# Optimization experiments

Measured on AMD Instinct MI355X. Metric: run time of the kernel, lower is better.

The kernel has to match this reference:

```python
import jax, jax.numpy as jnp
import numpy as np
from functools import partial

B, C, H, W = 16, 192, 32, 32
INNER, NH, DH, DCONV = 384, 12, 32, 4  # expand=2 -> INNER=2*C; 12 heads x 32 head_dim
S = H * W


def setup_inputs() -> dict:
    key = jax.random.key(0)
    ks = jax.random.split(key, 12)
    def n(k, shape, s=0.02):
        return jax.random.normal(k, shape, jnp.float32) * s
    f32 = jnp.float32
    return {
        "x": jax.random.normal(ks[0], (B, C, H, W), f32),
        "ln_w": jnp.ones((C,), f32), "ln_b": jnp.zeros((C,), f32),
        "w_up": n(ks[1], (C, 2 * INNER)), "b_up": jnp.zeros((2 * INNER,), f32),
        "conv_k": n(ks[2], (INNER, DCONV), 0.1), "conv_b": jnp.zeros((INNER,), f32),
        "w_q": n(ks[3], (INNER, INNER)), "w_k": n(ks[4], (INNER, INNER)),
        "w_i": n(ks[5], (3 * INNER, NH)), "b_i": jnp.zeros((NH,), f32),
        "w_f": n(ks[6], (3 * INNER, NH)), "b_f": 3.0 * jnp.ones((NH,), f32),
        "skip": jnp.ones((INNER,), f32),
        "mh_w": jnp.ones((INNER,), f32), "mh_b": jnp.zeros((INNER,), f32),
        "w_down": n(ks[7], (INNER, C)), "b_down": jnp.zeros((C,), f32),
        "w_lin": n(ks[8], (C, C)), "b_lin": jnp.zeros((C,), f32),
        "conv2_w": n(ks[9], (C, C, 3, 3), 0.05), "conv2_b": jnp.zeros((C,), f32),
        "bn_g": jnp.ones((C,), f32), "bn_b": jnp.zeros((C,), f32),
    }


def _layernorm(h, w, b, eps=1e-5):
    mu = h.mean(-1, keepdims=True)
    var = h.var(-1, keepdims=True)
    return (h - mu) / jnp.sqrt(var + eps) * w + b


def _mlstm_scan(q, k, v, i_pre, f_pre):
    # q,k,v: [B,S,NH,DH]; i_pre,f_pre: [B,S,NH]. Sequential matrix-memory mLSTM.
    qs, ks_, vs = (a.transpose(1, 0, 2, 3) for a in (q, k, v))  # seq-major
    iseq, fseq = i_pre.transpose(1, 0, 2), f_pre.transpose(1, 0, 2)

    def step(carry, inp):
        Cst, nst, mst = carry            # [B,NH,DH,DH], [B,NH,DH], [B,NH]
        qt, kt, vt, it, ft = inp
        log_f = jax.nn.log_sigmoid(ft)
        m_new = jnp.maximum(log_f + mst, it)
        f_s = jnp.exp(log_f + mst - m_new)[..., None]   # [B,NH,1]
        i_s = jnp.exp(it - m_new)[..., None]
        C_new = f_s[..., None] * Cst + i_s[..., None] * (vt[..., :, None] * kt[..., None, :])
        n_new = f_s * nst + i_s * kt
        denom = jnp.maximum(jnp.abs(jnp.einsum('bhd,bhd->bh', n_new, qt)), 1.0)[..., None]
        h = jnp.einsum('bhde,bhe->bhd', C_new, qt) / denom
        return (C_new, n_new, m_new), h

    bsz = q.shape[0]
    carry0 = (jnp.zeros((bsz, NH, DH, DH), q.dtype),
              jnp.zeros((bsz, NH, DH), q.dtype),
              jnp.zeros((bsz, NH), q.dtype))
    _, hs = jax.lax.scan(step, carry0, (qs, ks_, vs, iseq, fseq))
    return hs.transpose(1, 0, 2, 3)  # [B,S,NH,DH]


def _vil_block(seq, ln_w, ln_b, w_up, b_up, conv_k, conv_b, w_q, w_k,
               w_i, b_i, w_f, b_f, skip, mh_w, mh_b, w_down, b_down):
    # seq: [B,S,C]. Pre-norm mLSTM block (ViLBlock, rowwise-from-top-left order).
    bsz, s = seq.shape[0], seq.shape[1]
    h = _layernorm(seq, ln_w, ln_b)
    x_in, z = jnp.split(h @ w_up + b_up, 2, axis=-1)       # [B,S,INNER] each
    # causal depthwise conv1d, kernel DCONV
    x_pad = jnp.pad(x_in, ((0, 0), (DCONV - 1, 0), (0, 0)))
    x_conv = sum(x_pad[:, t:t + s, :] * conv_k[:, t] for t in range(DCONV)) + conv_b
    x_act = jax.nn.silu(x_conv)
    q = x_act @ w_q
    k = x_act @ w_k
    v = x_in
    gin = jnp.concatenate([q, k, v], -1)                    # [B,S,3*INNER]
    i_pre = gin @ w_i + b_i                                  # [B,S,NH]
    f_pre = gin @ w_f + b_f
    qh = q.reshape(bsz, s, NH, DH)
    kh = k.reshape(bsz, s, NH, DH) * (DH ** -0.5)
    vh = v.reshape(bsz, s, NH, DH)
    hs = _mlstm_scan(qh, kh, vh, i_pre, f_pre)              # [B,S,NH,DH]
    # per-head group norm
    mu = hs.mean(-1, keepdims=True)
    var = hs.var(-1, keepdims=True)
    hn = ((hs - mu) / jnp.sqrt(var + 1e-5)).reshape(bsz, s, INNER) * mh_w + mh_b
    h_out = (hn + skip * x_act) * jax.nn.silu(z)
    return seq + (h_out @ w_down + b_down)


def reference(x, ln_w, ln_b, w_up, b_up, conv_k, conv_b, w_q, w_k, w_i, b_i,
              w_f, b_f, skip, mh_w, mh_b, w_down, b_down, w_lin, b_lin,
              conv2_w, conv2_b, bn_g, bn_b):
    bsz, c, hh, ww = x.shape
    seq = x.reshape(bsz, c, hh * ww).transpose(0, 2, 1)     # [B,S,C]
    x1 = _vil_block(seq, ln_w, ln_b, w_up, b_up, conv_k, conv_b, w_q, w_k,
                    w_i, b_i, w_f, b_f, skip, mh_w, mh_b, w_down, b_down)
    x1 = x1.transpose(0, 2, 1).reshape(bsz, c, hh, ww)
    x2 = jax.nn.silu(seq @ w_lin + b_lin).transpose(0, 2, 1).reshape(bsz, c, hh, ww)
    y = x1 + x2
    y = jax.lax.conv_general_dilated(y, conv2_w, (1, 1), ((1, 1), (1, 1)),
                                     dimension_numbers=('NCHW', 'OIHW', 'NCHW'))
    y = y + conv2_b[None, :, None, None]
    # BatchNorm2d, training mode (batch statistics, biased variance)
    mu = y.mean((0, 2, 3), keepdims=True)
    var = y.var((0, 2, 3), keepdims=True)
    y = (y - mu) / jnp.sqrt(var + 1e-5) * bn_g[None, :, None, None] + bn_b[None, :, None, None]
    return jnp.where(y >= 0, y, 0.01 * y)  # LeakyReLU(0.01)
```

## Files before the change

kernel.cpp:

```cpp
#include <hip/hip_runtime.h>
#include <hip/hip_bf16.h>

#define BATCH 16
#define CDIM  192
#define SDIM  1024
#define INNER 384
#define NHEAD 12
#define DHEAD 32
#define UPN   768

typedef unsigned short ushort_t;
typedef __attribute__((ext_vector_type(8))) short bf16x8;
typedef __attribute__((ext_vector_type(4))) float f32x4;

__device__ __forceinline__ float us2f(ushort_t u) {
  union { unsigned int i; float f; } x; x.i = ((unsigned int)u) << 16; return x.f;
}
__device__ __forceinline__ float bits2f(unsigned int i) {
  union { unsigned int i; float f; } x; x.i = i; return x.f;
}
__device__ __forceinline__ ushort_t f2us(float f) {
  union { float f; unsigned int i; } x; x.f = f;
  unsigned int lsb = (x.i >> 16) & 1u;
  x.i += 0x7fffu + lsb;
  return (ushort_t)(x.i >> 16);
}
__device__ __forceinline__ void unpack8(uint4 u, float* o) {
  o[0] = bits2f(u.x << 16); o[1] = bits2f(u.x & 0xffff0000u);
  o[2] = bits2f(u.y << 16); o[3] = bits2f(u.y & 0xffff0000u);
  o[4] = bits2f(u.z << 16); o[5] = bits2f(u.z & 0xffff0000u);
  o[6] = bits2f(u.w << 16); o[7] = bits2f(u.w & 0xffff0000u);
}

__global__ void detect_kernel(const ushort_t* __restrict__ ln_w_raw,
                              int* __restrict__ flag) {
  if (threadIdx.x == 0) flag[0] = (ln_w_raw[0] == 0x3F80) ? 0 : 1;
}

#define NSEG 23
#define CANON_TOTAL 917600
struct CvtArgs { const void* src[NSEG]; };
__global__ __launch_bounds__(256) void convert_kernel(
    CvtArgs args, ushort_t* __restrict__ canon, const int* __restrict__ flagp) {
  const int offs[NSEG + 1] = {0, 192, 384, 147840, 148608, 150144, 150528,
      297984, 445440, 459264, 459280, 473104, 473120, 473504, 473888, 474272,
      548000, 548192, 585056, 585248, 917024, 917216, 917408, CANON_TOTAL};
  const int cnts[NSEG] = {192, 192, 147456, 768, 1536, 384, 147456, 147456,
      13824, 12, 13824, 12, 384, 384, 384, 73728, 192, 36864, 192, 331776,
      192, 192, 192};
  const int segK[NSEG] = {0,0,192,0,0,0,384,384,1152,0,1152,0,0,0,0,384,0,192,0,0,0,0,0};
  const int segN[NSEG] = {0,0,768,0,0,0,384,384,12,0,12,0,0,0,0,192,0,192,0,0,0,0,0};
  int idx = blockIdx.x * 256 + threadIdx.x;
  if (idx >= CANON_TOTAL) return;
  bool f32 = (*flagp) != 0;
  int seg = 0;
#pragma unroll
  for (int i = 1; i < NSEG; ++i) if (idx >= offs[i]) seg = i;
  int local = idx - offs[seg];
  ushort_t v = 0;
  if (local < cnts[seg]) {
    int srcidx = local;
    if (segK[seg] > 0) {
      int K = segK[seg], N = segN[seg];
      int n = local / K, k = local - n * K;
      srcidx = k * N + n;
    } else if (seg == 19) {
      int uv = local / 36864;
      int rem = local - uv * 36864;
      int co = rem / 192, ci = rem - co * 192;
      srcidx = (co * 192 + ci) * 9 + uv;
    }
    if (f32) v = f2us(((const float*)args.src[seg])[srcidx]);
    else     v = ((const ushort_t*)args.src[seg])[srcidx];
  }
  canon[idx] = v;
}

#define C_LN_W   0
#define C_LN_B   192
#define C_W_UP   384
#define C_B_UP   147840
#define C_CONV_K 148608
#define C_CONV_B 150144
#define C_W_Q    150528
#define C_W_K    297984
#define C_W_I    445440
#define C_B_I    459264
#define C_W_F    459280
#define C_B_F    473104
#define C_SKIP   473120
#define C_MH_W   473504
#define C_MH_B   473888
#define C_W_DOWN 474272
#define C_B_DOWN 548000
#define C_W_LIN  548192
#define C_B_LIN  585056
#define C_CONV2W 585248
#define C_CONV2B 917024
#define C_BN_G   917216
#define C_BN_B   917408

__global__ __launch_bounds__(256) void transpose_in_kernel(
    const void* __restrict__ xraw, ushort_t* __restrict__ seq,
    const int* __restrict__ flagp) {
  __shared__ ushort_t tile[32][33];
  bool f32 = (*flagp) != 0;
  int b = blockIdx.z, s0 = blockIdx.y * 32, c0 = blockIdx.x * 32;
  int tx = threadIdx.x, ty = threadIdx.y;
#pragma unroll
  for (int i = 0; i < 4; ++i) {
    int c = c0 + ty + i * 8;
    size_t idx = ((size_t)b * CDIM + c) * SDIM + s0 + tx;
    tile[ty + i * 8][tx] = f32 ? f2us(((const float*)xraw)[idx])
                               : ((const ushort_t*)xraw)[idx];
  }
  __syncthreads();
#pragma unroll
  for (int i = 0; i < 4; ++i) {
    int s = s0 + ty + i * 8;
    seq[((size_t)b * SDIM + s) * CDIM + c0 + tx] = tile[tx][ty + i * 8];
  }
}

__global__ __launch_bounds__(64) void ln_kernel(
    const ushort_t* __restrict__ seq, const ushort_t* __restrict__ w,
    const ushort_t* __restrict__ bias, ushort_t* __restrict__ hln) {
  size_t row = blockIdx.x;
  int lane = threadIdx.x;
  const ushort_t* p = seq + row * CDIM;
  float x0 = us2f(p[lane]), x1 = us2f(p[lane + 64]), x2 = us2f(p[lane + 128]);
  float s = x0 + x1 + x2;
#pragma unroll
  for (int off = 1; off <= 32; off <<= 1) s += __shfl_xor(s, off, 64);
  float mu = s * (1.0f / 192.0f);
  float d0 = x0 - mu, d1 = x1 - mu, d2 = x2 - mu;
  float sq = d0 * d0 + d1 * d1 + d2 * d2;
#pragma unroll
  for (int off = 1; off <= 32; off <<= 1) sq += __shfl_xor(sq, off, 64);
  float inv = rsqrtf(sq * (1.0f / 192.0f) + 1e-5f);
  ushort_t* o = hln + row * CDIM;
  o[lane]       = f2us(d0 * inv * us2f(w[lane])       + us2f(bias[lane]));
  o[lane + 64]  = f2us(d1 * inv * us2f(w[lane + 64])  + us2f(bias[lane + 64]));
  o[lane + 128] = f2us(d2 * inv * us2f(w[lane + 128]) + us2f(bias[lane + 128]));
}

#define GBK 32
#define LPAD 8
__global__ __launch_bounds__(256) void gemm_mfma(
    const ushort_t* __restrict__ A, int K,
    const ushort_t* __restrict__ Bt,
    float* Cf, ushort_t* Cb, int N,
    const ushort_t* __restrict__ bias,
    const ushort_t* add_bf, const float* add_f, int mode) {
  __shared__ ushort_t As[64][GBK + LPAD];
  __shared__ ushort_t Bs[64][GBK + LPAD];
  int tid = threadIdx.x;
  int wave = tid >> 6, lane = tid & 63;
  int m0 = blockIdx.y * 64, n0 = blockIdx.x * 64;
  int lr = tid >> 2;
  int lk = (tid & 3) * 8;
  int fr = lane & 15;
  int kq = (lane >> 4) * 8;
  f32x4 acc[4];
#pragma unroll
  for (int nt = 0; nt < 4; ++nt) acc[nt] = (f32x4){0.f, 0.f, 0.f, 0.f};
  const ushort_t* Ap = A + (size_t)(m0 + lr) * K + lk;
  const ushort_t* Bp = Bt + (size_t)(n0 + lr) * K + lk;
  for (int k0 = 0; k0 < K; k0 += GBK) {
    *(uint4*)&As[lr][lk] = *(const uint4*)(Ap + k0);
    *(uint4*)&Bs[lr][lk] = *(const uint4*)(Bp + k0);
    __syncthreads();
    bf16x8 af = *(const bf16x8*)&As[wave * 16 + fr][kq];
#pragma unroll
    for (int nt = 0; nt < 4; ++nt) {
      bf16x8 bf = *(const bf16x8*)&Bs[nt * 16 + fr][kq];
      acc[nt] = __builtin_amdgcn_mfma_f32_16x16x32_bf16(af, bf, acc[nt], 0, 0, 0);
    }
    __syncthreads();
  }
#pragma unroll
  for (int nt = 0; nt < 4; ++nt) {
    int col = n0 + nt * 16 + fr;
    float bv = bias ? us2f(bias[col]) : 0.0f;
#pragma unroll
    for (int r = 0; r < 4; ++r) {
      int row = m0 + wave * 16 + ((lane >> 4) << 2) + r;
      float v = acc[nt][r] + bv;
      if (mode == 1) {
        v = v / (1.0f + expf(-v));
      } else if (mode == 2) {
        size_t off = (size_t)row * N + col;
        v += us2f(add_bf[off]) + add_f[off];
      }
      if (Cb) Cb[(size_t)row * N + col] = f2us(v);
      else    Cf[(size_t)row * N + col] = v;
    }
  }
}

__global__ __launch_bounds__(256) void conv3_mfma_kernel(
    const ushort_t* __restrict__ ybsc, const ushort_t* __restrict__ w2t,
    const ushort_t* __restrict__ cbias, float* __restrict__ convo) {
  __shared__ ushort_t As[64][GBK + LPAD];
  __shared__ ushort_t Bs[64][GBK + LPAD];
  int tid = threadIdx.x;
  int wave = tid >> 6, lane = tid & 63;
  int n0 = blockIdx.x * 64;
  int my = blockIdx.y;
  int b = my >> 4;
  int m0 = (my & 15) * 64;
  int lr = tid >> 2, lk = (tid & 3) * 8;
  int fr = lane & 15, kq = (lane >> 4) * 8;
  f32x4 acc[4];
#pragma unroll
  for (int nt = 0; nt < 4; ++nt) acc[nt] = (f32x4){0.f, 0.f, 0.f, 0.f};
  int p = m0 + lr;
  int pi = p >> 5, pj = p & 31;
  const size_t brow = (size_t)b * SDIM;
#pragma unroll
  for (int uv = 0; uv < 9; ++uv) {
    int du = uv / 3 - 1, dv = uv % 3 - 1;
    bool valid = (pi + du >= 0) && (pi + du < 32) && (pj + dv >= 0) && (pj + dv < 32);
    const ushort_t* Ap = ybsc + (brow + p + du * 32 + dv) * CDIM + lk;
    const ushort_t* Bp = w2t + (size_t)uv * 36864 + (size_t)(n0 + lr) * CDIM + lk;
    for (int k0 = 0; k0 < CDIM; k0 += GBK) {
      uint4 av = {0u, 0u, 0u, 0u};
      if (valid) av = *(const uint4*)(Ap + k0);
      *(uint4*)&As[lr][lk] = av;
      *(uint4*)&Bs[lr][lk] = *(const uint4*)(Bp + k0);
      __syncthreads();
      bf16x8 af = *(const bf16x8*)&As[wave * 16 + fr][kq];
#pragma unroll
      for (int nt = 0; nt < 4; ++nt) {
        bf16x8 bf = *(const bf16x8*)&Bs[nt * 16 + fr][kq];
        acc[nt] = __builtin_amdgcn_mfma_f32_16x16x32_bf16(af, bf, acc[nt], 0, 0, 0);
      }
      __syncthreads();
    }
  }
#pragma unroll
  for (int nt = 0; nt < 4; ++nt) {
    int col = n0 + nt * 16 + fr;
    float bv = us2f(cbias[col]);
#pragma unroll
    for (int r = 0; r < 4; ++r) {
      int row = m0 + wave * 16 + ((lane >> 4) << 2) + r;
      convo[(brow + row) * CDIM + col] = acc[nt][r] + bv;
    }
  }
}

__global__ __launch_bounds__(256) void dwconv_kernel(
    const ushort_t* __restrict__ UPb, const ushort_t* __restrict__ ck,
    const ushort_t* __restrict__ cb, ushort_t* __restrict__ xact) {
  int idx = blockIdx.x * 256 + threadIdx.x;
  int ch = idx % INNER;
  int s = (idx / INNER) % SDIM;
  int b = idx / (INNER * SDIM);
  const ushort_t* p = UPb + ((size_t)b * SDIM + s) * UPN + ch;
  float acc = us2f(cb[ch]);
#pragma unroll
  for (int t = 0; t < 4; ++t) {
    int sp = s - 3 + t;
    if (sp >= 0) acc += us2f(p[(long)(t - 3) * UPN]) * us2f(ck[ch * 4 + t]);
  }
  xact[((size_t)b * SDIM + s) * INNER + ch] = f2us(acc / (1.0f + expf(-acc)));
}

__global__ __launch_bounds__(256) void gates_mfma_kernel(
    const ushort_t* __restrict__ qb, const ushort_t* __restrict__ kb,
    const ushort_t* __restrict__ UPb,
    const ushort_t* __restrict__ wiT, const ushort_t* __restrict__ b_i,
    const ushort_t* __restrict__ wfT, const ushort_t* __restrict__ b_f,
    float* __restrict__ ipre, float* __restrict__ fpre) {
  __shared__ ushort_t As[64][GBK + LPAD];
  __shared__ ushort_t Bs[32][GBK + LPAD];
  int tid = threadIdx.x;
  int wave = tid >> 6, lane = tid & 63;
  int m0 = blockIdx.x * 64;
  int lr = tid >> 2, lk = (tid & 3) * 8;
  int bn = tid >> 3, bk = (tid & 7) * 4;
  int fr = lane & 15, kq = (lane >> 4) * 8;
  f32x4 acc0 = (f32x4){0.f, 0.f, 0.f, 0.f};
  f32x4 acc1 = (f32x4){0.f, 0.f, 0.f, 0.f};
  for (int k0 = 0; k0 < 3 * INNER; k0 += GBK) {
    int reg = k0 / INNER;
    int off = k0 - reg * INNER + lk;
    const ushort_t* Ap;
    if (reg == 0)      Ap = qb + (size_t)(m0 + lr) * INNER + off;
    else if (reg == 1) Ap = kb + (size_t)(m0 + lr) * INNER + off;
    else               Ap = UPb + (size_t)(m0 + lr) * UPN + off;
    *(uint4*)&As[lr][lk] = *(const uint4*)Ap;
    ushort4 bv = {0, 0, 0, 0};
    if (bn < 12)       bv = *(const ushort4*)(wiT + (size_t)bn * 1152 + k0 + bk);
    else if (bn < 24)  bv = *(const ushort4*)(wfT + (size_t)(bn - 12) * 1152 + k0 + bk);
    *(ushort4*)&Bs[bn][bk] = bv;
    __syncthreads();
    bf16x8 af = *(const bf16x8*)&As[wave * 16 + fr][kq];
    bf16x8 bf0 = *(const bf16x8*)&Bs[fr][kq];
    acc0 = __builtin_amdgcn_mfma_f32_16x16x32_bf16(af, bf0, acc0, 0, 0, 0);
    bf16x8 bf1 = *(const bf16x8*)&Bs[16 + fr][kq];
    acc1 = __builtin_amdgcn_mfma_f32_16x16x32_bf16(af, bf1, acc1, 0, 0, 0);
    __syncthreads();
  }
#pragma unroll
  for (int r = 0; r < 4; ++r) {
    int row = m0 + wave * 16 + ((lane >> 4) << 2) + r;
    {
      int col = fr;
      float v = acc0[r];
      if (col < 12)      ipre[(size_t)row * NHEAD + col] = v + us2f(b_i[col]);
      else               fpre[(size_t)row * NHEAD + col - 12] = v + us2f(b_f[col - 12]);
    }
    {
      int col = 16 + fr;
      if (col < 24) fpre[(size_t)row * NHEAD + col - 12] = acc1[r] + us2f(b_f[col - 12]);
    }
  }
}

#define CHL 64
#define SAST 72

__global__ __launch_bounds__(256) void scanA_kernel(
    const ushort_t* __restrict__ qb, const ushort_t* __restrict__ kb,
    const ushort_t* __restrict__ UPb,
    const float* __restrict__ ipre, const float* __restrict__ fpre,
    ushort_t* __restrict__ hs, float* __restrict__ srowG,
    float* __restrict__ MlocG, float* __restrict__ sumG,
    ushort_t* __restrict__ CdG, ushort_t* __restrict__ ndG) {
  __shared__ ushort_t Qs[64 * SAST];
  __shared__ ushort_t Ks[64 * SAST];
  __shared__ ushort_t KtS[32 * SAST];
  __shared__ ushort_t VtS[48 * SAST];
  __shared__ ushort_t VwS[48 * SAST];
  __shared__ ushort_t Ss[64 * SAST];
  __shared__ float garr[CHL], Mloc_s[CHL], wlk_s[CHL];

  const int bx = blockIdx.x;
  const int bh = bx >> 4, c = bx & 15;
  const int b = bh / NHEAD, h = bh % NHEAD;
  const int tid = threadIdx.x;
  const int lane = tid & 63, wave = tid >> 6;
  const int quad = lane >> 4, fr = lane & 15;
  const int kq = quad * 8;
  const float kscale = 0.17677669529663687f;
  const size_t base384 = (size_t)b * SDIM * INNER + h * DHEAD;
  const size_t base768 = (size_t)b * SDIM * UPN + h * DHEAD;
  const size_t gbase = (size_t)b * SDIM * NHEAD + h;

  const int u = tid >> 2, dd0 = (tid & 3) * 8;
  size_t rb = base384 + (size_t)(c * CHL + u) * INNER + dd0;
  uint4 qv = *(const uint4*)(qb + rb);
  uint4 kv = *(const uint4*)(kb + rb);
  uint4 vv = *(const uint4*)(UPb + base768 + (size_t)(c * CHL + u) * UPN + dd0);
  *(uint4*)&Qs[u * SAST + dd0] = qv;
  *(uint4*)&Ks[u * SAST + dd0] = kv;
  {
    unsigned int words[4] = {kv.x, kv.y, kv.z, kv.w};
#pragma unroll
    for (int i = 0; i < 4; ++i) {
      KtS[(dd0 + 2 * i) * SAST + u] = (ushort_t)(words[i] & 0xffffu);
      KtS[(dd0 + 2 * i + 1) * SAST + u] = (ushort_t)(words[i] >> 16);
    }
  }
  if (tid < CHL) VtS[32 * SAST + tid] = 0x3F80;
  if (wave == 0) {
    float fv = fpre[gbase + (size_t)(c * CHL + lane) * NHEAD];
    float iv = ipre[gbase + (size_t)(c * CHL + lane) * NHEAD];
    float lf = fminf(fv, 0.0f) - log1pf(expf(-fabsf(fv)));
    float A = lf;
#pragma unroll
    for (int off = 1; off <= 32; off <<= 1) {
      float nb = __shfl_up(A, off, 64);
      if (lane >= off) A += nb;
    }
    float g = iv - A;
    float Mg = g;
#pragma unroll
    for (int off = 1; off <= 32; off <<= 1) {
      float nb = __shfl_up(Mg, off, 64);
      if (lane >= off) Mg = fmaxf(Mg, nb);
    }
    float Mg63 = __shfl(Mg, 63, 64);
    garr[lane] = g;
    Mloc_s[lane] = Mg;
    wlk_s[lane] = expf(g - Mg63) * kscale;
    MlocG[bx * CHL + lane] = Mg;
    if (lane == 63) { sumG[2 * bx] = A; sumG[2 * bx + 1] = Mg; }
  }
  __syncthreads();

  {
    float wk = wlk_s[u];
    unsigned int words[4] = {vv.x, vv.y, vv.z, vv.w};
#pragma unroll
    for (int i = 0; i < 4; ++i) {
      ushort_t lo = (ushort_t)(words[i] & 0xffffu);
      ushort_t hi = (ushort_t)(words[i] >> 16);
      VtS[(dd0 + 2 * i) * SAST + u] = lo;
      VtS[(dd0 + 2 * i + 1) * SAST + u] = hi;
      VwS[(dd0 + 2 * i) * SAST + u] = f2us(us2f(lo) * wk);
      VwS[(dd0 + 2 * i + 1) * SAST + u] = f2us(us2f(hi) * wk);
    }
    if (tid < CHL) VwS[32 * SAST + tid] = f2us(wlk_s[tid]);
  }
  f32x4 accS[4];
  {
    bf16x8 af = *(const bf16x8*)&Qs[(wave * 16 + fr) * SAST + kq];
#pragma unroll
    for (int nt = 0; nt < 4; ++nt) {
      bf16x8 bf = *(const bf16x8*)&Ks[(nt * 16 + fr) * SAST + kq];
      accS[nt] = __builtin_amdgcn_mfma_f32_16x16x32_bf16(
          af, bf, (f32x4){0.f, 0.f, 0.f, 0.f}, 0, 0, 0);
    }
  }
  {
    float Mls[4];
#pragma unroll
    for (int r = 0; r < 4; ++r) Mls[r] = Mloc_s[wave * 16 + quad * 4 + r];
#pragma unroll
    for (int nt = 0; nt < 4; ++nt) {
      int uu = nt * 16 + fr;
      float gu = garr[uu];
#pragma unroll
      for (int r = 0; r < 4; ++r) {
        int t = wave * 16 + quad * 4 + r;
        float sv = (uu <= t) ? accS[nt][r] * kscale * expf(gu - Mls[r]) : 0.0f;
        Ss[t * SAST + uu] = f2us(sv);
      }
    }
  }
  __syncthreads();

  f32x4 acc2[3];
#pragma unroll
  for (int nt = 0; nt < 3; ++nt) acc2[nt] = (f32x4){0.f, 0.f, 0.f, 0.f};
#pragma unroll
  for (int ks = 0; ks < 2; ++ks) {
    bf16x8 af = *(const bf16x8*)&Ss[(wave * 16 + fr) * SAST + kq + 32 * ks];
#pragma unroll
    for (int nt = 0; nt < 3; ++nt) {
      bf16x8 bf = *(const bf16x8*)&VtS[(nt * 16 + fr) * SAST + kq + 32 * ks];
      acc2[nt] = __builtin_amdgcn_mfma_f32_16x16x32_bf16(af, bf, acc2[nt], 0, 0, 0);
    }
  }
  f32x4 accC[2];
  const int nC = (wave < 2) ? 2 : 1;
#pragma unroll
  for (int tt = 0; tt < 2; ++tt) {
    if (tt < nC) {
      int tix = wave + tt * 4;
      int m = tix >> 1, n = tix & 1;
      f32x4 a = (f32x4){0.f, 0.f, 0.f, 0.f};
#pragma unroll
      for (int ks = 0; ks < 2; ++ks) {
        bf16x8 af = *(const bf16x8*)&VwS[(m * 16 + fr) * SAST + kq + 32 * ks];
        bf16x8 bf = *(const bf16x8*)&KtS[(n * 16 + fr) * SAST + kq + 32 * ks];
        a = __builtin_amdgcn_mfma_f32_16x16x32_bf16(af, bf, a, 0, 0, 0);
      }
      accC[tt] = a;
    }
  }
#pragma unroll
  for (int r = 0; r < 4; ++r) {
    int t = wave * 16 + quad * 4 + r;
    size_t hrow = base384 + (size_t)(c * CHL + t) * INNER;
    hs[hrow + fr] = f2us(acc2[0][r]);
    hs[hrow + 16 + fr] = f2us(acc2[1][r]);
    if (fr == 0) srowG[bx * CHL + t] = acc2[2][r];
  }
#pragma unroll
  for (int tt = 0; tt < 2; ++tt) {
    if (tt < nC) {
      int tix = wave + tt * 4;
      int m = tix >> 1, n = tix & 1;
#pragma unroll
      for (int r = 0; r < 4; ++r) {
        int dp = m * 16 + quad * 4 + r;
        int e = n * 16 + fr;
        if (dp < 32)       CdG[(size_t)bx * 1024 + dp * 32 + e] = f2us(accC[tt][r]);
        else if (dp == 32) ndG[bx * 32 + e] = f2us(accC[tt][r]);
      }
    }
  }
}

__global__ __launch_bounds__(256) void scanB_kernel(
    ushort_t* __restrict__ CdG, ushort_t* __restrict__ ndG,
    float* __restrict__ sumG) {
  __shared__ float Cl[DHEAD][33];
  __shared__ float nl[DHEAD];
  const int bh = blockIdx.x;
  const int tid = threadIdx.x;
  const int d = tid & 31, e0 = tid >> 5;
  Cl[d][e0] = 0.0f; Cl[d][e0 + 8] = 0.0f;
  Cl[d][e0 + 16] = 0.0f; Cl[d][e0 + 24] = 0.0f;
  if (tid < DHEAD) nl[tid] = 0.0f;
  float m = 0.0f;
  __syncthreads();
  for (int c = 0; c < 16; ++c) {
    int bx = bh * 16 + c;
    float A63 = sumG[2 * bx], Mg63 = sumG[2 * bx + 1];
    ushort_t* Cd = CdG + (size_t)bx * 1024 + d * 32;
    float d0 = us2f(Cd[e0]), d1 = us2f(Cd[e0 + 8]);
    float d2 = us2f(Cd[e0 + 16]), d3 = us2f(Cd[e0 + 24]);
    float ndel = (tid < DHEAD) ? us2f(ndG[bx * 32 + tid]) : 0.0f;
    __syncthreads();
    Cd[e0] = f2us(Cl[d][e0]); Cd[e0 + 8] = f2us(Cl[d][e0 + 8]);
    Cd[e0 + 16] = f2us(Cl[d][e0 + 16]); Cd[e0 + 24] = f2us(Cl[d][e0 + 24]);
    if (tid < DHEAD) ndG[bx * 32 + tid] = f2us(nl[tid]);
    if (tid == 0) sumG[2 * bx] = m;
    float M63 = fmaxf(m, Mg63);
    float al = expf(m - M63), sc = expf(Mg63 - M63);
    Cl[d][e0] = al * Cl[d][e0] + sc * d0;
    Cl[d][e0 + 8] = al * Cl[d][e0 + 8] + sc * d1;
    Cl[d][e0 + 16] = al * Cl[d][e0 + 16] + sc * d2;
    Cl[d][e0 + 24] = al * Cl[d][e0 + 24] + sc * d3;
    if (tid < DHEAD) nl[tid] = al * nl[tid] + sc * ndel;
    m = A63 + M63;
    __syncthreads();
  }
}

__global__ __launch_bounds__(256) void scanC_kernel(
    const ushort_t* __restrict__ qb, const ushort_t* __restrict__ CdG,
    const ushort_t* __restrict__ ndG, const float* __restrict__ sumG,
    const float* __restrict__ srowG, const float* __restrict__ MlocG,
    ushort_t* __restrict__ hs) {
  __shared__ ushort_t Qs[64 * SAST];
  __shared__ ushort_t Bs2[48 * 40];
  __shared__ float als[CHL], scs[CHL], rden[CHL];
  __shared__ float mprev_s;
  const int bx = blockIdx.x;
  const int bh = bx >> 4, c = bx & 15;
  const int b = bh / NHEAD, h = bh % NHEAD;
  const int tid = threadIdx.x;
  const int lane = tid & 63, wave = tid >> 6;
  const int quad = lane >> 4, fr = lane & 15;
  const int kq = quad * 8;
  const size_t base384 = (size_t)b * SDIM * INNER + h * DHEAD;
  {
    int u = tid >> 2, dd0 = (tid & 3) * 8;
    size_t rb = base384 + (size_t)(c * CHL + u) * INNER + dd0;
    *(uint4*)&Qs[u * SAST + dd0] = *(const uint4*)(qb + rb);
  }
  if (tid < 128) {
    int d = tid >> 2, e0 = (tid & 3) * 8;
    *(uint4*)&Bs2[d * 40 + e0] =
        *(const uint4*)(CdG + (size_t)bx * 1024 + d * 32 + e0);
  } else if (tid < 160) {
    Bs2[32 * 40 + (tid - 128)] = ndG[bx * 32 + (tid - 128)];
  } else if (tid == 160) {
    mprev_s = sumG[2 * bx];
  }
  __syncthreads();
  f32x4 acc[3];
  {
    bf16x8 af = *(const bf16x8*)&Qs[(wave * 16 + fr) * SAST + kq];
#pragma unroll
    for (int nt = 0; nt < 3; ++nt) {
      bf16x8 bf = *(const bf16x8*)&Bs2[(nt * 16 + fr) * 40 + kq];
      acc[nt] = __builtin_amdgcn_mfma_f32_16x16x32_bf16(
          af, bf, (f32x4){0.f, 0.f, 0.f, 0.f}, 0, 0, 0);
    }
  }
  float mp = mprev_s;
  if (fr == 0) {
#pragma unroll
    for (int r = 0; r < 4; ++r) {
      int t = wave * 16 + quad * 4 + r;
      float Mloc = MlocG[bx * CHL + t];
      float srow = srowG[bx * CHL + t];
      float Mt = fmaxf(mp, Mloc);
      float al = expf(mp - Mt), sc = expf(Mloc - Mt);
      float ndot = al * acc[2][r] + sc * srow;
      als[t] = al; scs[t] = sc;
      rden[t] = 1.0f / fmaxf(fabsf(ndot), 1.0f);
    }
  }
  __syncthreads();
#pragma unroll
  for (int r = 0; r < 4; ++r) {
    int t = wave * 16 + quad * 4 + r;
    float al = als[t], sc = scs[t], rd = rden[t];
    size_t hrow = base384 + (size_t)(c * CHL + t) * INNER;
#pragma unroll
    for (int nt = 0; nt < 2; ++nt) {
      size_t off = hrow + nt * 16 + fr;
      float intra = us2f(hs[off]);
      hs[off] = f2us((al * acc[nt][r] + sc * intra) * rd);
    }
  }
}

__global__ __launch_bounds__(384) void gnorm_kernel(
    ushort_t* __restrict__ hs, const ushort_t* __restrict__ xact,
    const ushort_t* __restrict__ UPb, const ushort_t* __restrict__ mh_w,
    const ushort_t* __restrict__ mh_b, const ushort_t* __restrict__ skip) {
  size_t row = blockIdx.x;
  int t = threadIdx.x;
  float val = us2f(hs[row * INNER + t]);
  float s = val;
#pragma unroll
  for (int off = 1; off <= 16; off <<= 1) s += __shfl_xor(s, off, 64);
  float mu = s * (1.0f / 32.0f);
  float d = val - mu;
  float sq = d * d;
#pragma unroll
  for (int off = 1; off <= 16; off <<= 1) sq += __shfl_xor(sq, off, 64);
  float var = sq * (1.0f / 32.0f);
  float hn = d * rsqrtf(var + 1e-5f) * us2f(mh_w[t]) + us2f(mh_b[t]);
  float xa = us2f(xact[row * INNER + t]);
  float z = us2f(UPb[row * UPN + INNER + t]);
  float sz = z / (1.0f + expf(-z));
  hs[row * INNER + t] = f2us((hn + us2f(skip[t]) * xa) * sz);
}

__global__ __launch_bounds__(192) void bnpart_kernel(
    const float* __restrict__ convo, float* __restrict__ part) {
  int blk = blockIdx.x;
  int c = threadIdx.x;
  float s = 0.0f, s2 = 0.0f;
  const float* p = convo + (size_t)blk * 64 * CDIM + c;
  for (int r = 0; r < 64; ++r) {
    float v = p[(size_t)r * CDIM];
    s += v; s2 += v * v;
  }
  part[blk * 384 + c] = s;
  part[blk * 384 + 192 + c] = s2;
}

__global__ __launch_bounds__(192) void bnreduce_kernel(
    const float* __restrict__ part, float* __restrict__ stats) {
  int c = threadIdx.x;
  double s = 0.0, s2 = 0.0;
  for (int b = 0; b < 256; ++b) {
    s += (double)part[b * 384 + c];
    s2 += (double)part[b * 384 + 192 + c];
  }
  double mu = s * (1.0 / 16384.0);
  double var = s2 * (1.0 / 16384.0) - mu * mu;
  if (var < 0.0) var = 0.0;
  stats[2 * c] = (float)mu;
  stats[2 * c + 1] = (float)(1.0 / sqrt(var + 1e-5));
}

__global__ __launch_bounds__(256) void bnapply_t_kernel(
    const float* __restrict__ convo, const float* __restrict__ stats,
    const ushort_t* __restrict__ g, const ushort_t* __restrict__ bb,
    void* __restrict__ out, const int* __restrict__ flagp) {
  __shared__ float tile[32][33];
  int b = blockIdx.z, s0 = blockIdx.y * 32, c0 = blockIdx.x * 32;
  int tx = threadIdx.x, ty = threadIdx.y;
  int c = c0 + tx;
  float mu = stats[2 * c], inv = stats[2 * c + 1];
  float gg = us2f(g[c]), bv = us2f(bb[c]);
#pragma unroll
  for (int i = 0; i < 4; ++i) {
    int s = s0 + ty + i * 8;
    float v = convo[((size_t)b * SDIM + s) * CDIM + c];
    v = (v - mu) * inv * gg + bv;
    v = v >= 0.0f ? v : 0.01f * v;
    tile[ty + i * 8][tx] = v;
  }
  __syncthreads();
  bool f32o = (*flagp) != 0;
#pragma unroll
  for (int i = 0; i < 4; ++i) {
    int cc = c0 + ty + i * 8;
    float v = tile[tx][ty + i * 8];
    size_t oidx = ((size_t)b * CDIM + cc) * SDIM + s0 + tx;
    if (f32o) ((float*)out)[oidx] = v;
    else      ((ushort_t*)out)[oidx] = f2us(v);
  }
}

extern "C" void kernel_launch(void* const* d_in, const int* in_sizes, int n_in,
                              void* d_out, int out_size, void* d_ws, size_t ws_size,
                              hipStream_t stream) {
  (void)in_sizes; (void)n_in; (void)out_size; (void)ws_size;
  char* w = (char*)d_ws;
  ushort_t* seqb  = (ushort_t*)(w + 0);
  ushort_t* hlnb  = (ushort_t*)(w + 6291456);
  ushort_t* UPb   = (ushort_t*)(w + 12582912);
  ushort_t* xactb = (ushort_t*)(w + 37748736);
  ushort_t* qbb   = (ushort_t*)(w + 50331648);
  ushort_t* kbb   = (ushort_t*)(w + 62914560);
  ushort_t* hsb   = (ushort_t*)(w + 75497472);
  float* ipre     = (float*)(w + 88080384);
  float* fpre     = (float*)(w + 88866816);
  float* stats    = (float*)(w + 89653248);
  int* flag       = (int*)(w + 89654784);
  ushort_t* canon = (ushort_t*)(w + 89654848);
  float* srowG    = (float*)(w + 91490048);
  float* MlocG    = (float*)(w + 92276480);
  float* sumG     = (float*)(w + 93062912);
  ushort_t* CdG   = (ushort_t*)(w + 93087488);
  ushort_t* ndG   = (ushort_t*)(w + 99378944);
  float* x2f      = (float*)xactb;
  ushort_t* ybscb = hlnb;
  float* convo    = (float*)qbb;
  float* part     = (float*)kbb;

  const ushort_t* ln_w   = canon + C_LN_W;
  const ushort_t* ln_b   = canon + C_LN_B;
  const ushort_t* w_upT  = canon + C_W_UP;
  const ushort_t* b_up   = canon + C_B_UP;
  const ushort_t* conv_k = canon + C_CONV_K;
  const ushort_t* conv_b = canon + C_CONV_B;
  const ushort_t* w_qT   = canon + C_W_Q;
  const ushort_t* w_kT   = canon + C_W_K;
  const ushort_t* w_iT   = canon + C_W_I;
  const ushort_t* b_i    = canon + C_B_I;
  const ushort_t* w_fT   = canon + C_W_F;
  const ushort_t* b_f    = canon + C_B_F;
  const ushort_t* skip   = canon + C_SKIP;
  const ushort_t* mh_w   = canon + C_MH_W;
  const ushort_t* mh_b   = canon + C_MH_B;
  const ushort_t* w_downT= canon + C_W_DOWN;
  const ushort_t* b_down = canon + C_B_DOWN;
  const ushort_t* w_linT = canon + C_W_LIN;
  const ushort_t* b_lin  = canon + C_B_LIN;
  const ushort_t* conv2w = canon + C_CONV2W;
  const ushort_t* conv2b = canon + C_CONV2B;
  const ushort_t* bn_g   = canon + C_BN_G;
  const ushort_t* bn_b   = canon + C_BN_B;

  detect_kernel<<<1, 64, 0, stream>>>((const ushort_t*)d_in[1], flag);
  CvtArgs ca;
  for (int i = 0; i < NSEG; ++i) ca.src[i] = d_in[i + 1];
  convert_kernel<<<(CANON_TOTAL + 255) / 256, 256, 0, stream>>>(ca, canon, flag);

  transpose_in_kernel<<<dim3(6, 32, 16), dim3(32, 8), 0, stream>>>(d_in[0], seqb, flag);
  ln_kernel<<<16384, 64, 0, stream>>>(seqb, ln_w, ln_b, hlnb);
  gemm_mfma<<<dim3(12, 256), 256, 0, stream>>>(hlnb, CDIM, w_upT, nullptr, UPb,
                                               UPN, b_up, nullptr, nullptr, 0);
  dwconv_kernel<<<24576, 256, 0, stream>>>(UPb, conv_k, conv_b, xactb);
  gemm_mfma<<<dim3(6, 256), 256, 0, stream>>>(xactb, INNER, w_qT, nullptr, qbb,
                                              INNER, nullptr, nullptr, nullptr, 0);
  gemm_mfma<<<dim3(6, 256), 256, 0, stream>>>(xactb, INNER, w_kT, nullptr, kbb,
                                              INNER, nullptr, nullptr, nullptr, 0);
  gates_mfma_kernel<<<256, 256, 0, stream>>>(qbb, kbb, UPb, w_iT, b_i, w_fT, b_f,
                                             ipre, fpre);
  scanA_kernel<<<3072, 256, 0, stream>>>(qbb, kbb, UPb, ipre, fpre, hsb,
                                         srowG, MlocG, sumG, CdG, ndG);
  scanB_kernel<<<192, 256, 0, stream>>>(CdG, ndG, sumG);
  scanC_kernel<<<3072, 256, 0, stream>>>(qbb, CdG, ndG, sumG, srowG, MlocG, hsb);
  gnorm_kernel<<<16384, 384, 0, stream>>>(hsb, xactb, UPb, mh_w, mh_b, skip);
  gemm_mfma<<<dim3(3, 256), 256, 0, stream>>>(seqb, CDIM, w_linT, x2f, nullptr,
                                              CDIM, b_lin, nullptr, nullptr, 1);
  gemm_mfma<<<dim3(3, 256), 256, 0, stream>>>(hsb, INNER, w_downT, nullptr, ybscb,
                                              CDIM, b_down, seqb, x2f, 2);
  conv3_mfma_kernel<<<dim3(3, 256), 256, 0, stream>>>(ybscb, conv2w, conv2b, convo);
  bnpart_kernel<<<256, 192, 0, stream>>>(convo, part);
  bnreduce_kernel<<<1, 192, 0, stream>>>(part, stats);
  bnapply_t_kernel<<<dim3(6, 32, 16), dim3(32, 8), 0, stream>>>(convo, stats, bn_g,
                                                                bn_b, d_out, flag);
}
```

Before: 390.4 us.

## Fuse Q/K GEMMs, fold group-norm into scanC, merge lin and down GEMMs

Three fusions. The separate Q and K projection GEMMs become one launch that splits output columns between the two buffers. The per-row head group-norm, skip and SiLU gating move into scanC's epilogue using shuffle reductions, which removes the gnorm kernel and its extra read/write of hs. The SiLU linear branch and the down projection are computed in one kernel with two accumulators, which removes the fp32 x2f intermediate buffer. The Q/K fusion assumes w_q and w_k are stored contiguously in the canonical weight buffer.

Measured after the change: 364.9 us. -6.5%, faster.

```diff
diff --git a/kernel.cpp b/kernel.cpp
--- a/kernel.cpp
+++ b/kernel.cpp
@@ -149,9 +149,8 @@
 __global__ __launch_bounds__(256) void gemm_mfma(
     const ushort_t* __restrict__ A, int K,
     const ushort_t* __restrict__ Bt,
-    float* Cf, ushort_t* Cb, int N,
-    const ushort_t* __restrict__ bias,
-    const ushort_t* add_bf, const float* add_f, int mode) {
+    ushort_t* Cb, ushort_t* Cb2, int splitN, int N,
+    const ushort_t* __restrict__ bias) {
   __shared__ ushort_t As[64][GBK + LPAD];
   __shared__ ushort_t Bs[64][GBK + LPAD];
   int tid = threadIdx.x;
@@ -182,18 +181,78 @@
   for (int nt = 0; nt < 4; ++nt) {
     int col = n0 + nt * 16 + fr;
     float bv = bias ? us2f(bias[col]) : 0.0f;
+    ushort_t* dst = Cb;
+    int c2 = col;
+    if (col >= splitN) { dst = Cb2; c2 = col - splitN; }
 #pragma unroll
     for (int r = 0; r < 4; ++r) {
       int row = m0 + wave * 16 + ((lane >> 4) << 2) + r;
-      float v = acc[nt][r] + bv;
-      if (mode == 1) {
-        v = v / (1.0f + expf(-v));
-      } else if (mode == 2) {
-        size_t off = (size_t)row * N + col;
-        v += us2f(add_bf[off]) + add_f[off];
+      dst[(size_t)row * N + c2] = f2us(acc[nt][r] + bv);
+    }
+  }
+}
+
+__global__ __launch_bounds__(256) void gemm_lindown(
+    const ushort_t* __restrict__ seq, const ushort_t* __restrict__ hsb,
+    const ushort_t* __restrict__ wlinT, const ushort_t* __restrict__ b_lin,
+    const ushort_t* __restrict__ wdownT, const ushort_t* __restrict__ b_down,
+    ushort_t* __restrict__ out) {
+  __shared__ ushort_t As[64][GBK + LPAD];
+  __shared__ ushort_t Bs[64][GBK + LPAD];
+  int tid = threadIdx.x;
+  int wave = tid >> 6, lane = tid & 63;
+  int m0 = blockIdx.y * 64, n0 = blockIdx.x * 64;
+  int lr = tid >> 2, lk = (tid & 3) * 8;
+  int fr = lane & 15, kq = (lane >> 4) * 8;
+  f32x4 accL[4], accD[4];
+#pragma unroll
+  for (int nt = 0; nt < 4; ++nt) {
+    accL[nt] = (f32x4){0.f, 0.f, 0.f, 0.f};
+    accD[nt] = (f32x4){0.f, 0.f, 0.f, 0.f};
+  }
+  {
+    const ushort_t* Ap = seq + (size_t)(m0 + lr) * CDIM + lk;
+    const ushort_t* Bp = wlinT + (size_t)(n0 + lr) * CDIM + lk;
+    for (int k0 = 0; k0 < CDIM; k0 += GBK) {
+      *(uint4*)&As[lr][lk] = *(const uint4*)(Ap + k0);
+      *(uint4*)&Bs[lr][lk] = *(const uint4*)(Bp + k0);
+      __syncthreads();
+      bf16x8 af = *(const bf16x8*)&As[wave * 16 + fr][kq];
+#pragma unroll
+      for (int nt = 0; nt < 4; ++nt) {
+        bf16x8 bf = *(const bf16x8*)&Bs[nt * 16 + fr][kq];
+        accL[nt] = __builtin_amdgcn_mfma_f32_16x16x32_bf16(af, bf, accL[nt], 0, 0, 0);
       }
-      if (Cb) Cb[(size_t)row * N + col] = f2us(v);
-      else    Cf[(size_t)row * N + col] = v;
+      __syncthreads();
+    }
+  }
+  {
+    const ushort_t* Ap = hsb + (size_t)(m0 + lr) * INNER + lk;
+    const ushort_t* Bp = wdownT + (size_t)(n0 + lr) * INNER + lk;
+    for (int k0 = 0; k0 < INNER; k0 += GBK) {
+      *(uint4*)&As[lr][lk] = *(const uint4*)(Ap + k0);
+      *(uint4*)&Bs[lr][lk] = *(const uint4*)(Bp + k0);
+      __syncthreads();
+      bf16x8 af = *(const bf16x8*)&As[wave * 16 + fr][kq];
+#pragma unroll
+      for (int nt = 0; nt < 4; ++nt) {
+        bf16x8 bf = *(const bf16x8*)&Bs[nt * 16 + fr][kq];
+        accD[nt] = __builtin_amdgcn_mfma_f32_16x16x32_bf16(af, bf, accD[nt], 0, 0, 0);
+      }
+      __syncthreads();
+    }
+  }
+#pragma unroll
+  for (int nt = 0; nt < 4; ++nt) {
+    int col = n0 + nt * 16 + fr;
+    float bl = us2f(b_lin[col]), bd = us2f(b_down[col]);
+#pragma unroll
+    for (int r = 0; r < 4; ++r) {
+      int row = m0 + wave * 16 + ((lane >> 4) << 2) + r;
+      float sl = accL[nt][r] + bl;
+      sl = sl / (1.0f + expf(-sl));
+      float v = accD[nt][r] + bd + us2f(seq[(size_t)row * CDIM + col]) + sl;
+      out[(size_t)row * CDIM + col] = f2us(v);
     }
   }
 }
@@ -527,7 +586,9 @@
     const ushort_t* __restrict__ qb, const ushort_t* __restrict__ CdG,
     const ushort_t* __restrict__ ndG, const float* __restrict__ sumG,
     const float* __restrict__ srowG, const float* __restrict__ MlocG,
-    ushort_t* __restrict__ hs) {
+    ushort_t* __restrict__ hs, const ushort_t* __restrict__ xact,
+    const ushort_t* __restrict__ UPb, const ushort_t* __restrict__ mh_w,
+    const ushort_t* __restrict__ mh_b, const ushort_t* __restrict__ skipw) {
   __shared__ ushort_t Qs[64 * SAST];
   __shared__ ushort_t Bs2[48 * 40];
   __shared__ float als[CHL], scs[CHL], rden[CHL];
@@ -540,6 +601,7 @@
   const int quad = lane >> 4, fr = lane & 15;
   const int kq = quad * 8;
   const size_t base384 = (size_t)b * SDIM * INNER + h * DHEAD;
+  const size_t zbase = (size_t)b * SDIM * UPN + INNER + h * DHEAD;
   {
     int u = tid >> 2, dd0 = (tid & 3) * 8;
     size_t rb = base384 + (size_t)(c * CHL + u) * INNER + dd0;
@@ -580,41 +642,37 @@
     }
   }
   __syncthreads();
+  float w0 = us2f(mh_w[h * 32 + fr]), w1 = us2f(mh_w[h * 32 + 16 + fr]);
+  float bb0 = us2f(mh_b[h * 32 + fr]), bb1 = us2f(mh_b[h * 32 + 16 + fr]);
+  float sk0 = us2f(skipw[h * 32 + fr]), sk1 = us2f(skipw[h * 32 + 16 + fr]);
 #pragma unroll
   for (int r = 0; r < 4; ++r) {
     int t = wave * 16 + quad * 4 + r;
     float al = als[t], sc = scs[t], rd = rden[t];
     size_t hrow = base384 + (size_t)(c * CHL + t) * INNER;
-#pragma unroll
-    for (int nt = 0; nt < 2; ++nt) {
-      size_t off = hrow + nt * 16 + fr;
-      float intra = us2f(hs[off]);
-      hs[off] = f2us((al * acc[nt][r] + sc * intra) * rd);
-    }
-  }
-}
-
-__global__ __launch_bounds__(384) void gnorm_kernel(
-    ushort_t* __restrict__ hs, const ushort_t* __restrict__ xact,
-    const ushort_t* __restrict__ UPb, const ushort_t* __restrict__ mh_w,
-    const ushort_t* __restrict__ mh_b, const ushort_t* __restrict__ skip) {
-  size_t row = blockIdx.x;
-  int t = threadIdx.x;
-  float val = us2f(hs[row * INNER + t]);
-  float s = val;
-#pragma unroll
-  for (int off = 1; off <= 16; off <<= 1) s += __shfl_xor(s, off, 64);
-  float mu = s * (1.0f / 32.0f);
-  float d = val - mu;
-  float sq = d * d;
-#pragma unroll
-  for (int off = 1; off <= 16; off <<= 1) sq += __shfl_xor(sq, off, 64);
-  float var = sq * (1.0f / 32.0f);
-  float hn = d * rsqrtf(var + 1e-5f) * us2f(mh_w[t]) + us2f(mh_b[t]);
-  float xa = us2f(xact[row * INNER + t]);
-  float z = us2f(UPb[row * UPN + INNER + t]);
-  float sz = z / (1.0f + expf(-z));
-  hs[row * INNER + t] = f2us((hn + us2f(skip[t]) * xa) * sz);
+    float h0 = (al * acc[0][r] + sc * us2f(hs[hrow + fr])) * rd;
+    float h1 = (al * acc[1][r] + sc * us2f(hs[hrow + 16 + fr])) * rd;
+    float s = h0 + h1;
+#pragma unroll
+    for (int off = 1; off <= 8; off <<= 1) s += __shfl_xor(s, off, 64);
+    float mu = s * (1.0f / 32.0f);
+    float d0 = h0 - mu, d1 = h1 - mu;
+    float sq = d0 * d0 + d1 * d1;
+#pragma unroll
+    for (int off = 1; off <= 8; off <<= 1) sq += __shfl_xor(sq, off, 64);
+    float inv = rsqrtf(sq * (1.0f / 32.0f) + 1e-5f);
+    float hn0 = d0 * inv * w0 + bb0;
+    float hn1 = d1 * inv * w1 + bb1;
+    float xa0 = us2f(xact[hrow + fr]);
+    float xa1 = us2f(xact[hrow + 16 + fr]);
+    size_t zrow = zbase + (size_t)(c * CHL + t) * UPN;
+    float z0 = us2f(UPb[zrow + fr]);
+    float z1 = us2f(UPb[zrow + 16 + fr]);
+    float g0 = (hn0 + sk0 * xa0) * (z0 / (1.0f + expf(-z0)));
+    float g1 = (hn1 + sk1 * xa1) * (z1 / (1.0f + expf(-z1)));
+    hs[hrow + fr] = f2us(g0);
+    hs[hrow + 16 + fr] = f2us(g1);
+  }
 }
 
 __global__ __launch_bounds__(192) void bnpart_kernel(
@@ -698,7 +756,6 @@
   float* sumG     = (float*)(w + 93062912);
   ushort_t* CdG   = (ushort_t*)(w + 93087488);
   ushort_t* ndG   = (ushort_t*)(w + 99378944);
-  float* x2f      = (float*)xactb;
   ushort_t* ybscb = hlnb;
   float* convo    = (float*)qbb;
   float* part     = (float*)kbb;
@@ -709,13 +766,12 @@
   const ushort_t* b_up   = canon + C_B_UP;
   const ushort_t* conv_k = canon + C_CONV_K;
   const ushort_t* conv_b = canon + C_CONV_B;
-  const ushort_t* w_qT   = canon + C_W_Q;
-  const ushort_t* w_kT   = canon + C_W_K;
+  const ushort_t* w_qkT  = canon + C_W_Q;
   const ushort_t* w_iT   = canon + C_W_I;
   const ushort_t* b_i    = canon + C_B_I;
   const ushort_t* w_fT   = canon + C_W_F;
   const ushort_t* b_f    = canon + C_B_F;
-  const ushort_t* skip   = canon + C_SKIP;
+  const ushort_t* skipw  = canon + C_SKIP;
   const ushort_t* mh_w   = canon + C_MH_W;
   const ushort_t* mh_b   = canon + C_MH_B;
   const ushort_t* w_downT= canon + C_W_DOWN;
@@ -734,24 +790,20 @@
 
   transpose_in_kernel<<<dim3(6, 32, 16), dim3(32, 8), 0, stream>>>(d_in[0], seqb, flag);
   ln_kernel<<<16384, 64, 0, stream>>>(seqb, ln_w, ln_b, hlnb);
-  gemm_mfma<<<dim3(12, 256), 256, 0, stream>>>(hlnb, CDIM, w_upT, nullptr, UPb,
-                                               UPN, b_up, nullptr, nullptr, 0);
+  gemm_mfma<<<dim3(12, 256), 256, 0, stream>>>(hlnb, CDIM, w_upT, UPb, nullptr,
+                                               0x7fffffff, UPN, b_up);
   dwconv_kernel<<<24576, 256, 0, stream>>>(UPb, conv_k, conv_b, xactb);
-  gemm_mfma<<<dim3(6, 256), 256, 0, stream>>>(xactb, INNER, w_qT, nullptr, qbb,
-                                              INNER, nullptr, nullptr, nullptr, 0);
-  gemm_mfma<<<dim3(6, 256), 256, 0, stream>>>(xactb, INNER, w_kT, nullptr, kbb,
-                                              INNER, nullptr, nullptr, nullptr, 0);
+  gemm_mfma<<<dim3(12, 256), 256, 0, stream>>>(xactb, INNER, w_qkT, qbb, kbb,
+                                               384, INNER, nullptr);
   gates_mfma_kernel<<<256, 256, 0, stream>>>(qbb, kbb, UPb, w_iT, b_i, w_fT, b_f,
                                              ipre, fpre);
   scanA_kernel<<<3072, 256, 0, stream>>>(qbb, kbb, UPb, ipre, fpre, hsb,
                                          srowG, MlocG, sumG, CdG, ndG);
   scanB_kernel<<<192, 256, 0, stream>>>(CdG, ndG, sumG);
-  scanC_kernel<<<3072, 256, 0, stream>>>(qbb, CdG, ndG, sumG, srowG, MlocG, hsb);
-  gnorm_kernel<<<16384, 384, 0, stream>>>(hsb, xactb, UPb, mh_w, mh_b, skip);
-  gemm_mfma<<<dim3(3, 256), 256, 0, stream>>>(seqb, CDIM, w_linT, x2f, nullptr,
-                                              CDIM, b_lin, nullptr, nullptr, 1);
-  gemm_mfma<<<dim3(3, 256), 256, 0, stream>>>(hsb, INNER, w_downT, nullptr, ybscb,
-                                              CDIM, b_down, seqb, x2f, 2);
+  scanC_kernel<<<3072, 256, 0, stream>>>(qbb, CdG, ndG, sumG, srowG, MlocG, hsb,
+                                         xactb, UPb, mh_w, mh_b, skipw);
+  gemm_lindown<<<dim3(3, 256), 256, 0, stream>>>(seqb, hsb, w_linT, b_lin,
+                                                 w_downT, b_down, ybscb);
   conv3_mfma_kernel<<<dim3(3, 256), 256, 0, stream>>>(ybscb, conv2w, conv2b, convo);
   bnpart_kernel<<<256, 192, 0, stream>>>(convo, part);
   bnreduce_kernel<<<1, 192, 0, stream>>>(part, stats);
```
